# Optimization experiments

Hardware: AMD Instinct MI355X
Metric: run time of the kernel (lower is better)

## Reference

```python
import jax, jax.numpy as jnp
import numpy as np

B, T, E = 8, 1024, 512
H = 1024            # hidden_dim
NH, QD, VD = 4, 256, 512
C1, C2 = 512, 2     # conv1_out, conv2_out
K, PAD = 3, 1


def conv1d(x, w, b, pad):
    # x: [B, Cin, T], w: [Cout, Cin, K]
    y = jax.lax.conv_general_dilated(x, w, (1,), [(pad, pad)],
                                     dimension_numbers=('NCH', 'OIH', 'NCH'))
    return y + b[None, :, None]


def setup_inputs() -> dict:
    key = jax.random.key(0)
    ks = jax.random.split(key, 24)
    n = lambda i, shape, s=0.02: jax.random.normal(ks[i], shape, dtype=jnp.float32) * s
    inp = {
        'x':    jax.random.normal(ks[0], (B, T, E), dtype=jnp.float32),
        # in_pro: two 1x1 convs over channels (acting as linears)
        'w_in1': n(1, (E, E)), 'b_in1': jnp.zeros((E,), jnp.float32),
        'w_in2': n(2, (E, E)), 'b_in2': jnp.zeros((E,), jnp.float32),
        # attention projections
        'w_q': n(3, (NH * QD, E), float(np.sqrt(2.0 / (E + QD)))), 'b_q': jnp.zeros((NH * QD,), jnp.float32),
        'w_k': n(4, (NH * QD, E), float(np.sqrt(2.0 / (E + QD)))), 'b_k': jnp.zeros((NH * QD,), jnp.float32),
        'w_v': n(5, (NH * VD, E), float(np.sqrt(2.0 / (E + VD)))), 'b_v': jnp.zeros((NH * VD,), jnp.float32),
        # output projection (1x1 conv)
        'w_p': n(6, (E, NH * VD)), 'b_p': jnp.zeros((E,), jnp.float32),
        # layernorm
        'ln_g': jnp.ones((E,), jnp.float32), 'ln_b': jnp.zeros((E,), jnp.float32),
        # LSTM (1 layer, unidirectional, hidden H)
        'w_ih': n(7, (4 * H, E)), 'w_hh': n(8, (4 * H, H)),
        'b_ih': jnp.zeros((4 * H,), jnp.float32), 'b_hh': jnp.zeros((4 * H,), jnp.float32),
        # attention pooling convs
        'w_c1': n(9, (C1, H, K)), 'b_c1': jnp.zeros((C1,), jnp.float32),
        'w_c2': n(10, (C2, C1, K)), 'b_c2': jnp.zeros((C2,), jnp.float32),
    }
    return inp


def reference(x, w_in1, b_in1, w_in2, b_in2, w_q, b_q, w_k, b_k, w_v, b_v,
              w_p, b_p, ln_g, ln_b, w_ih, w_hh, b_ih, b_hh,
              w_c1, b_c1, w_c2, b_c2):
    # in_pro: 1x1 conv -> LeakyReLU(0.25) -> 1x1 conv (channel-wise linears)
    h = jnp.einsum('bte,fe->btf', x, w_in1) + b_in1
    h = jnp.where(h >= 0, h, 0.25 * h)
    h = jnp.einsum('bte,fe->btf', h, w_in2) + b_in2  # [B,T,E]

    # multi-head attention (no scale factor, as in the source)
    q = (jnp.einsum('bte,fe->btf', h, w_q) + b_q).reshape(B, T, NH, QD)
    k = (jnp.einsum('bte,fe->btf', h, w_k) + b_k).reshape(B, T, NH, QD)
    v = (jnp.einsum('bte,fe->btf', h, w_v) + b_v).reshape(B, T, NH, VD)
    scores = jnp.einsum('btnd,bsnd->bnts', q, k)          # [B,NH,T,T]
    attn = jax.nn.softmax(scores, axis=-1)
    o = jnp.einsum('bnts,bsnd->btnd', attn, v)            # [B,T,NH,VD]
    o = o.reshape(B, T, NH * VD)

    # p_conv1 (1x1) then LayerNorm over E
    y = jnp.einsum('btc,ec->bte', o, w_p) + b_p           # [B,T,E]
    mu = jnp.mean(y, axis=-1, keepdims=True)
    var = jnp.mean(jnp.square(y - mu), axis=-1, keepdims=True)
    y = (y - mu) * jax.lax.rsqrt(var + 1e-5) * ln_g + ln_b

    # LSTM (batch_first, 1 layer); dropout is identity in eval mode
    def step(carry, xt):
        hprev, cprev = carry
        g = xt @ w_ih.T + hprev @ w_hh.T + b_ih + b_hh    # [B,4H]
        i, f, gg, og = jnp.split(g, 4, axis=-1)
        c = jax.nn.sigmoid(f) * cprev + jax.nn.sigmoid(i) * jnp.tanh(gg)
        hn = jax.nn.sigmoid(og) * jnp.tanh(c)
        return (hn, c), hn
    init = (jnp.zeros((B, H), y.dtype), jnp.zeros((B, H), y.dtype))
    _, hs = jax.lax.scan(step, init, jnp.swapaxes(y, 0, 1))  # [T,B,H]
    lstm_out = jnp.swapaxes(hs, 0, 1)                        # [B,T,H]

    # conv-based attention pooling
    a = conv1d(jnp.swapaxes(lstm_out, 1, 2), w_c1, b_c1, PAD)  # [B,C1,T]
    a = jax.nn.relu(a)
    a = conv1d(a, w_c2, b_c2, PAD)                              # [B,C2,T]
    a = jax.nn.softmax(a, axis=2)
    feat = jnp.einsum('bct,bth->bch', a, lstm_out)              # [B,C2,H]
    return feat.reshape(B, C2 * H)
```

## Files before the change

### kernel.cpp

```cpp
#include <hip/hip_runtime.h>
#include <stdint.h>

typedef short short8 __attribute__((ext_vector_type(8)));
typedef short short4v __attribute__((ext_vector_type(4)));
typedef float float4v __attribute__((ext_vector_type(4)));

__device__ __forceinline__ float b2f(short s) {
    return __uint_as_float(((unsigned)(unsigned short)s) << 16);
}
__device__ __forceinline__ short f2b(float f) {
    unsigned u = __float_as_uint(f);
    unsigned r = (u + 0x7fffu + ((u >> 16) & 1u)) >> 16;
    return (short)r;
}

__global__ void k_cvt_all(const float4v* __restrict__ xs,
                          const float4v* __restrict__ s0, const float4v* __restrict__ s1,
                          const float4v* __restrict__ s2, const float4v* __restrict__ s3,
                          const float4v* __restrict__ s4, const float4v* __restrict__ s5,
                          const float4v* __restrict__ s6, const float4v* __restrict__ s7,
                          short4v* __restrict__ xq, short4v* __restrict__ wq) {
    int i = blockIdx.x * blockDim.x + threadIdx.x;
    int stride = gridDim.x * blockDim.x;
    for (; i < 3538944; i += stride) {
        float4v v;
        short4v* dst;
        int di;
        if (i < 1048576) { v = xs[i]; dst = xq; di = i; }
        else {
            int j = i - 1048576;
            dst = wq; di = j;
            if      (j <   65536) v = s0[j];
            else if (j <  131072) v = s1[j -   65536];
            else if (j <  262144) v = s2[j -  131072];
            else if (j <  393216) v = s3[j -  262144];
            else if (j <  655360) v = s4[j -  393216];
            else if (j <  917504) v = s5[j -  655360];
            else if (j < 1441792) v = s6[j -  917504];
            else                  v = s7[j - 1441792];
        }
        short4v o;
        o[0] = f2b(v[0]); o[1] = f2b(v[1]); o[2] = f2b(v[2]); o[3] = f2b(v[3]);
        dst[di] = o;
    }
}

__global__ void k_small_prep(const float* __restrict__ wc1, short* __restrict__ wc1b,
                             const float* __restrict__ bih, const float* __restrict__ bhh,
                             float* __restrict__ bsum, short* __restrict__ lpad,
                             short* __restrict__ hs0, short* __restrict__ hs1,
                             int* __restrict__ arr) {
    int t0 = blockIdx.x * blockDim.x + threadIdx.x;
    int stride = gridDim.x * blockDim.x;
    for (int i = t0; i < 512 * 3072; i += stride) {
        int c = i / 3072, rr = i % 3072, dk = rr / 1024, h = rr % 1024;
        wc1b[i] = f2b(wc1[(c * 1024 + h) * 3 + dk]);
    }
    for (int i = t0; i < 4096; i += stride) bsum[i] = bih[i] + bhh[i];
    for (int i = t0; i < 16 * 1024; i += stride) {
        int b = i >> 11, r = (i >> 10) & 1, h = i & 1023;
        lpad[((long)(b * 1026 + r * 1025)) * 1024 + h] = 0;
    }
    for (int i = t0; i < 16384; i += stride) { hs0[i] = 0; hs1[i] = 0; }
    for (int i = t0; i < 128; i += stride) arr[i] = 0;
}

__global__ __launch_bounds__(256) void k_gemm_bt(
    const short* __restrict__ A, const short* __restrict__ B,
    float* __restrict__ Cf, short* __restrict__ Cb,
    const float* __restrict__ bias,
    int M, int N, int K, int lda, int ldb, int ldc,
    int z0n, long sA0, long sA1, long sB0, long sB1, long sC0, long sC1,
    int act, int gap)
{
    __shared__ __align__(16) short lds[2 * 128 * 32];
    const int z = blockIdx.z;
    const int z0 = z % z0n, z1 = z / z0n;
    A += z1 * sA1 + z0 * sA0;
    B += z1 * sB1 + z0 * sB0;
    const long coff = z1 * sC1 + z0 * sC0;
    const int tn0 = blockIdx.x * 128, tm0 = blockIdx.y * 128;
    const int tid = threadIdx.x, ln = tid & 63, wv = tid >> 6;
    const int wr = wv >> 1, wc = wv & 1;

    const short* gbase[4];
    {
        const int gcol = (ln & 3) ^ ((ln >> 3) & 3);
#pragma unroll
        for (int j = 0; j < 4; ++j) {
            int c = wv * 4 + j;
            if (c < 8) {
                long grow = (long)(tm0 + c * 16 + (ln >> 2));
                if (gap) grow += 2 * (grow >> 10);
                gbase[j] = A + grow * (long)lda + gcol * 8;
            } else {
                gbase[j] = B + (long)(tn0 + (c - 8) * 16 + (ln >> 2)) * ldb + gcol * 8;
            }
        }
    }

    float4v acc[4][4];
#pragma unroll
    for (int i = 0; i < 4; ++i)
#pragma unroll
        for (int j = 0; j < 4; ++j) acc[i][j] = (float4v){0.f, 0.f, 0.f, 0.f};

    const int nk = K >> 5;
    for (int kt = 0; kt < nk; ++kt) {
        __syncthreads();
#pragma unroll
        for (int j = 0; j < 4; ++j) {
            int c = wv * 4 + j;
            __builtin_amdgcn_global_load_lds(
                (const __attribute__((address_space(1))) void*)(gbase[j] + kt * 32),
                (__attribute__((address_space(3))) void*)((short8*)lds + c * 64),
                16, 0, 0);
        }
        __syncthreads();

        short8 af[4], bf_[4];
        const int q = ln >> 4;
#pragma unroll
        for (int i = 0; i < 4; ++i) {
            int r = wr * 64 + i * 16 + (ln & 15);
            af[i] = ((short8*)lds)[r * 4 + (q ^ ((r >> 1) & 3))];
        }
#pragma unroll
        for (int j = 0; j < 4; ++j) {
            int r = wc * 64 + j * 16 + (ln & 15);
            bf_[j] = ((short8*)lds)[512 + r * 4 + (q ^ ((r >> 1) & 3))];
        }
#pragma unroll
        for (int i = 0; i < 4; ++i)
#pragma unroll
            for (int j = 0; j < 4; ++j)
                acc[i][j] = __builtin_amdgcn_mfma_f32_16x16x32_bf16(af[i], bf_[j], acc[i][j], 0, 0, 0);
    }

#pragma unroll
    for (int j = 0; j < 4; ++j) {
        int nglob = tn0 + wc * 64 + j * 16 + (ln & 15);
        float bv = bias ? bias[nglob] : 0.f;
#pragma unroll
        for (int i = 0; i < 4; ++i) {
#pragma unroll
            for (int r = 0; r < 4; ++r) {
                int mglob = tm0 + wr * 64 + i * 16 + (ln >> 4) * 4 + r;
                float v = acc[i][j][r] + bv;
                if (act == 1) v = (v >= 0.f) ? v : 0.25f * v;
                else if (act == 2) v = fmaxf(v, 0.f);
                long ci = coff + (long)mglob * ldc + nglob;
                if (Cf) Cf[ci] = v;
                if (Cb) Cb[ci] = f2b(v);
            }
        }
    }
}

__global__ __launch_bounds__(256) void k_gemm_bt64(
    const short* __restrict__ A, const short* __restrict__ B,
    float* __restrict__ Cf, short* __restrict__ Cb,
    const float* __restrict__ bias,
    int M, int N, int K, int lda, int ldb, int ldc,
    int z0n, long sA0, long sA1, long sB0, long sB1, long sC0, long sC1,
    int act, int gap)
{
    __shared__ __align__(16) short lds[(64 + 128) * 32];
    const int z = blockIdx.z;
    const int z0 = z % z0n, z1 = z / z0n;
    A += z1 * sA1 + z0 * sA0;
    B += z1 * sB1 + z0 * sB0;
    const long coff = z1 * sC1 + z0 * sC0;
    const int tn0 = blockIdx.x * 128, tm0 = blockIdx.y * 64;
    const int tid = threadIdx.x, ln = tid & 63, wv = tid >> 6;
    const int wr = wv >> 1, wc = wv & 1;

    const short* gbase[3];
    {
        const int gcol = (ln & 3) ^ ((ln >> 3) & 3);
#pragma unroll
        for (int j = 0; j < 3; ++j) {
            int c = wv * 3 + j;
            if (c < 4) {
                long grow = (long)(tm0 + c * 16 + (ln >> 2));
                if (gap) grow += 2 * (grow >> 10);
                gbase[j] = A + grow * (long)lda + gcol * 8;
            } else {
                gbase[j] = B + (long)(tn0 + (c - 4) * 16 + (ln >> 2)) * ldb + gcol * 8;
            }
        }
    }

    float4v acc[2][4];
#pragma unroll
    for (int i = 0; i < 2; ++i)
#pragma unroll
        for (int j = 0; j < 4; ++j) acc[i][j] = (float4v){0.f, 0.f, 0.f, 0.f};

    const int nk = K >> 5;
    for (int kt = 0; kt < nk; ++kt) {
        __syncthreads();
#pragma unroll
        for (int j = 0; j < 3; ++j) {
            int c = wv * 3 + j;
            __builtin_amdgcn_global_load_lds(
                (const __attribute__((address_space(1))) void*)(gbase[j] + kt * 32),
                (__attribute__((address_space(3))) void*)((short8*)lds + c * 64),
                16, 0, 0);
        }
        __syncthreads();

        short8 af[2], bf_[4];
        const int q = ln >> 4;
#pragma unroll
        for (int i = 0; i < 2; ++i) {
            int r = wr * 32 + i * 16 + (ln & 15);
            af[i] = ((short8*)lds)[r * 4 + (q ^ ((r >> 1) & 3))];
        }
#pragma unroll
        for (int j = 0; j < 4; ++j) {
            int r = wc * 64 + j * 16 + (ln & 15);
            bf_[j] = ((short8*)lds)[256 + r * 4 + (q ^ ((r >> 1) & 3))];
        }
#pragma unroll
        for (int i = 0; i < 2; ++i)
#pragma unroll
            for (int j = 0; j < 4; ++j)
                acc[i][j] = __builtin_amdgcn_mfma_f32_16x16x32_bf16(af[i], bf_[j], acc[i][j], 0, 0, 0);
    }

#pragma unroll
    for (int j = 0; j < 4; ++j) {
        int nglob = tn0 + wc * 64 + j * 16 + (ln & 15);
        float bv = bias ? bias[nglob] : 0.f;
#pragma unroll
        for (int i = 0; i < 2; ++i) {
#pragma unroll
            for (int r = 0; r < 4; ++r) {
                int mglob = tm0 + wr * 32 + i * 16 + (ln >> 4) * 4 + r;
                float v = acc[i][j][r] + bv;
                if (act == 1) v = (v >= 0.f) ? v : 0.25f * v;
                else if (act == 2) v = fmaxf(v, 0.f);
                long ci = coff + (long)mglob * ldc + nglob;
                if (Cf) Cf[ci] = v;
                if (Cb) Cb[ci] = f2b(v);
            }
        }
    }
}

__global__ __launch_bounds__(256) void k_softmax_rows_bf16(short* __restrict__ p) {
    long row = blockIdx.x;
    short* r = p + (row << 10);
    int tid = threadIdx.x;
    float v[4];
    float mx = -3.4e38f;
#pragma unroll
    for (int i = 0; i < 4; ++i) { v[i] = b2f(r[tid + (i << 8)]); mx = fmaxf(mx, v[i]); }
#pragma unroll
    for (int d = 32; d > 0; d >>= 1) mx = fmaxf(mx, __shfl_down(mx, d));
    __shared__ float red[4], red2[4];
    if ((tid & 63) == 0) red[tid >> 6] = mx;
    __syncthreads();
    mx = fmaxf(fmaxf(red[0], red[1]), fmaxf(red[2], red[3]));
    float s = 0.f;
#pragma unroll
    for (int i = 0; i < 4; ++i) { v[i] = __expf(v[i] - mx); s += v[i]; }
#pragma unroll
    for (int d = 32; d > 0; d >>= 1) s += __shfl_down(s, d);
    if ((tid & 63) == 0) red2[tid >> 6] = s;
    __syncthreads();
    s = red2[0] + red2[1] + red2[2] + red2[3];
    float inv = 1.f / s;
#pragma unroll
    for (int i = 0; i < 4; ++i) r[tid + (i << 8)] = f2b(v[i] * inv);
}

__global__ __launch_bounds__(256) void k_layernorm(const short* __restrict__ y,
                                                   const float* __restrict__ gam,
                                                   const float* __restrict__ bet,
                                                   short* __restrict__ o) {
    const long row = blockIdx.x;
    const short* r = y + (row << 9);
    const int tid = threadIdx.x;
    float v0 = b2f(r[tid]), v1 = b2f(r[tid + 256]);
    float s = v0 + v1, ss = v0 * v0 + v1 * v1;
#pragma unroll
    for (int d = 32; d > 0; d >>= 1) { s += __shfl_down(s, d); ss += __shfl_down(ss, d); }
    __shared__ float rs_[4], rss[4];
    if ((tid & 63) == 0) { rs_[tid >> 6] = s; rss[tid >> 6] = ss; }
    __syncthreads();
    s = rs_[0] + rs_[1] + rs_[2] + rs_[3];
    ss = rss[0] + rss[1] + rss[2] + rss[3];
    float mean = s * (1.f / 512.f);
    float var = ss * (1.f / 512.f) - mean * mean;
    float rstd = rsqrtf(var + 1e-5f);
    short* out = o + (row << 9);
    out[tid]       = f2b((v0 - mean) * rstd * gam[tid]       + bet[tid]);
    out[tid + 256] = f2b((v1 - mean) * rstd * gam[tid + 256] + bet[tid + 256]);
}

__global__ __launch_bounds__(256) void k_vT(const short* __restrict__ v, short* __restrict__ vT) {
    __shared__ short t[32][34];
    int bn = blockIdx.z, b = bn >> 2, n = bn & 3;
    int s0 = blockIdx.y * 32, d0 = blockIdx.x * 32;
    int lx = threadIdx.x & 31, ly = threadIdx.x >> 5;
#pragma unroll
    for (int i = 0; i < 4; ++i) {
        int s = ly + i * 8;
        t[s][lx] = v[(long)(b * 1024 + s0 + s) * 2048 + n * 512 + d0 + lx];
    }
    __syncthreads();
#pragma unroll
    for (int i = 0; i < 4; ++i) {
        int d = ly + i * 8;
        vT[((long)bn * 512 + d0 + d) * 1024 + s0 + lx] = t[lx][d];
    }
}

__global__ __launch_bounds__(256) void k_lstm(
    const short* __restrict__ whh, const short* __restrict__ igb,
    short* __restrict__ hA, short* __restrict__ hB,
    short* __restrict__ lstm_pad, int* __restrict__ arr)
{
    const int g = blockIdx.x;
    const int tid = threadIdx.x;
    const int ln = tid & 63, wv = tid >> 6;
    const int kbase = wv * 256 + ((ln >> 4) << 3);
    const int arow = ln & 15;

    short8 wf[4][8];
#pragma unroll
    for (int q = 0; q < 4; ++q) {
        long row = (long)q * 1024 + g * 16 + (ln & 15);
#pragma unroll
        for (int kk = 0; kk < 8; ++kk)
            wf[q][kk] = *(const short8*)&whh[row * 1024 + kbase + kk * 32];
    }

    __shared__ float part[4][16][68];
    const int gm = tid >> 4, gu = tid & 15;
    float c_prev = 0.f;
    float igv[4];
    if (tid < 128) {
#pragma unroll
        for (int q = 0; q < 4; ++q)
            igv[q] = b2f(igb[((long)gm * 1024 + 0) * 4096 + q * 1024 + g * 16 + gu]);
    }

    for (int step = 0; step < 1024; ++step) {
        const short* hp = (step & 1) ? hB : hA;
        short8 af[8];
        if (arow < 8) {
            const unsigned long long* hq =
                (const unsigned long long*)(hp + arow * 1024 + kbase);
#pragma unroll
            for (int kk = 0; kk < 8; ++kk) {
                union { unsigned long long u[2]; short8 s; } cv;
                cv.u[0] = __hip_atomic_load(hq + kk * 8,     __ATOMIC_RELAXED, __HIP_MEMORY_SCOPE_AGENT);
                cv.u[1] = __hip_atomic_load(hq + kk * 8 + 1, __ATOMIC_RELAXED, __HIP_MEMORY_SCOPE_AGENT);
                af[kk] = cv.s;
            }
        } else {
#pragma unroll
            for (int kk = 0; kk < 8; ++kk) af[kk] = (short8){0, 0, 0, 0, 0, 0, 0, 0};
        }

        float4v acc[4];
#pragma unroll
        for (int q = 0; q < 4; ++q) acc[q] = (float4v){0.f, 0.f, 0.f, 0.f};
#pragma unroll
        for (int kk = 0; kk < 8; ++kk)
#pragma unroll
            for (int q = 0; q < 4; ++q)
                acc[q] = __builtin_amdgcn_mfma_f32_16x16x32_bf16(af[kk], wf[q][kk], acc[q], 0, 0, 0);

#pragma unroll
        for (int q = 0; q < 4; ++q)
#pragma unroll
            for (int rr = 0; rr < 4; ++rr)
                part[wv][(ln >> 4) * 4 + rr][q * 16 + (ln & 15)] = acc[q][rr];
        __syncthreads();

        if (tid < 128) {
            float psum[4];
#pragma unroll
            for (int q = 0; q < 4; ++q)
                psum[q] = part[0][gm][q * 16 + gu] + part[1][gm][q * 16 + gu]
                        + part[2][gm][q * 16 + gu] + part[3][gm][q * 16 + gu];
            float g0 = psum[0] + igv[0];
            float g1 = psum[1] + igv[1];
            float g2 = psum[2] + igv[2];
            float g3 = psum[3] + igv[3];
            float iv = 1.f / (1.f + __expf(-g0));
            float fv = 1.f / (1.f + __expf(-g1));
            float gv = 2.f / (1.f + __expf(-2.f * g2)) - 1.f;
            float ov = 1.f / (1.f + __expf(-g3));
            float c = fv * c_prev + iv * gv;
            c_prev = c;
            float h = ov * (2.f / (1.f + __expf(-2.f * c)) - 1.f);
            short hb16 = f2b(h);
            short* hn = (step & 1) ? hA : hB;
            __hip_atomic_store(&hn[gm * 1024 + g * 16 + gu], hb16,
                               __ATOMIC_RELAXED, __HIP_MEMORY_SCOPE_AGENT);
            lstm_pad[((long)gm * 1026 + step + 1) * 1024 + g * 16 + gu] = hb16;
        }

        __syncthreads();
        if (tid == 0)
            __hip_atomic_store(&arr[g], step + 1, __ATOMIC_RELAXED, __HIP_MEMORY_SCOPE_AGENT);
        if (tid < 128 && step + 1 < 1024) {
#pragma unroll
            for (int q = 0; q < 4; ++q)
                igv[q] = b2f(igb[((long)gm * 1024 + step + 1) * 4096 + q * 1024 + g * 16 + gu]);
        }
        if (wv == 0) {
            const int target = step + 1;
            long att = 0;
            while (true) {
                int f0 = __hip_atomic_load(&arr[ln], __ATOMIC_RELAXED, __HIP_MEMORY_SCOPE_AGENT);
                if (__all(f0 >= target)) break;
                if (++att > 20000000L) break;
                __builtin_amdgcn_s_sleep(1);
            }
        }
        __syncthreads();
    }
}

__global__ __launch_bounds__(256) void k_conv2(const short* __restrict__ a1,
                                               const float* __restrict__ w,
                                               const float* __restrict__ bias,
                                               float* __restrict__ a2) {
    __shared__ float wl[1536];
    int blk = blockIdx.x;
    int b = blk >> 3, c = (blk >> 2) & 1, t0 = (blk & 3) * 256;
    int tid = threadIdx.x;
    for (int i = tid; i < 1536; i += 256) wl[i] = w[c * 1536 + i];
    __syncthreads();
    int t = t0 + tid;
    float s = bias[c];
    for (int dk = 0; dk < 3; ++dk) {
        int tt = t + dk - 1;
        if (tt < 0 || tt >= 1024) continue;
        const short8* arow = (const short8*)(a1 + (long)(b * 1024 + tt) * 512);
#pragma unroll 4
        for (int j = 0; j < 64; ++j) {
            short8 v = arow[j];
#pragma unroll
            for (int u = 0; u < 8; ++u)
                s += b2f(v[u]) * wl[(j * 8 + u) * 3 + dk];
        }
    }
    a2[(b * 2 + c) * 1024 + t] = s;
}

__global__ __launch_bounds__(256) void k_feat(const float* __restrict__ a2,
                                              const short* __restrict__ lstm_pad,
                                              float* __restrict__ out) {
    int blk = blockIdx.x;
    int bc = blk >> 2, qh = blk & 3;
    int b = bc >> 1;
    int tid = threadIdx.x;
    int h = qh * 256 + tid;
    __shared__ float aw[1024];
    __shared__ float red[4], red2[4];
    float v[4];
    float mx = -3.4e38f;
#pragma unroll
    for (int i = 0; i < 4; ++i) { v[i] = a2[bc * 1024 + tid + (i << 8)]; mx = fmaxf(mx, v[i]); }
#pragma unroll
    for (int d = 32; d > 0; d >>= 1) mx = fmaxf(mx, __shfl_down(mx, d));
    if ((tid & 63) == 0) red[tid >> 6] = mx;
    __syncthreads();
    mx = fmaxf(fmaxf(red[0], red[1]), fmaxf(red[2], red[3]));
    float s = 0.f;
#pragma unroll
    for (int i = 0; i < 4; ++i) { v[i] = __expf(v[i] - mx); s += v[i]; }
#pragma unroll
    for (int d = 32; d > 0; d >>= 1) s += __shfl_down(s, d);
    if ((tid & 63) == 0) red2[tid >> 6] = s;
    __syncthreads();
    s = red2[0] + red2[1] + red2[2] + red2[3];
    float inv = 1.f / s;
#pragma unroll
    for (int i = 0; i < 4; ++i) aw[tid + (i << 8)] = v[i] * inv;
    __syncthreads();
    float acc = 0.f;
#pragma unroll 16
    for (int t = 0; t < 1024; ++t)
        acc += aw[t] * b2f(lstm_pad[((long)(b * 1026 + t + 1)) * 1024 + h]);
    out[bc * 1024 + h] = acc;
}

static void gemm_bt(hipStream_t st, const short* A, const short* B, float* Cf, short* Cb,
                    const float* bias, int M, int N, int K, int lda, int ldb, int ldc,
                    int z, int z0n, long sA0, long sA1, long sB0, long sB1, long sC0, long sC1,
                    int act, int gap) {
    dim3 grid(N / 128, M / 128, z);
    k_gemm_bt<<<grid, dim3(256), 0, st>>>(A, B, Cf, Cb, bias, M, N, K, lda, ldb, ldc,
                                          z0n, sA0, sA1, sB0, sB1, sC0, sC1, act, gap);
}

static void gemm_bt64(hipStream_t st, const short* A, const short* B, float* Cf, short* Cb,
                      const float* bias, int M, int N, int K, int lda, int ldb, int ldc,
                      int z, int z0n, long sA0, long sA1, long sB0, long sB1, long sC0, long sC1,
                      int act, int gap) {
    dim3 grid(N / 128, M / 64, z);
    k_gemm_bt64<<<grid, dim3(256), 0, st>>>(A, B, Cf, Cb, bias, M, N, K, lda, ldb, ldc,
                                            z0n, sA0, sA1, sB0, sB1, sC0, sC1, act, gap);
}

extern "C" void kernel_launch(void* const* d_in, const int* in_sizes, int n_in,
                              void* d_out, int out_size, void* d_ws, size_t ws_size,
                              hipStream_t stream) {
    if (ws_size < 199409920u) return;

    const float* x     = (const float*)d_in[0];
    const float* w_in1 = (const float*)d_in[1];
    const float* b_in1 = (const float*)d_in[2];
    const float* w_in2 = (const float*)d_in[3];
    const float* b_in2 = (const float*)d_in[4];
    const float* w_q   = (const float*)d_in[5];
    const float* b_q   = (const float*)d_in[6];
    const float* w_k   = (const float*)d_in[7];
    const float* b_k   = (const float*)d_in[8];
    const float* w_v   = (const float*)d_in[9];
    const float* b_v   = (const float*)d_in[10];
    const float* w_p   = (const float*)d_in[11];
    const float* b_p   = (const float*)d_in[12];
    const float* ln_g  = (const float*)d_in[13];
    const float* ln_b  = (const float*)d_in[14];
    const float* w_ih  = (const float*)d_in[15];
    const float* w_hh  = (const float*)d_in[16];
    const float* b_ih  = (const float*)d_in[17];
    const float* b_hh  = (const float*)d_in[18];
    const float* w_c1  = (const float*)d_in[19];
    const float* b_c1  = (const float*)d_in[20];
    const float* w_c2  = (const float*)d_in[21];
    const float* b_c2  = (const float*)d_in[22];

    char* ws = (char*)d_ws;
    short* w1b  = (short*)(ws + 0);
    short* w2b  = (short*)(ws + 524288);
    short* wqb  = (short*)(ws + 1048576);
    short* wkb  = (short*)(ws + 2097152);
    short* wvb  = (short*)(ws + 3145728);
    short* wpb  = (short*)(ws + 5242880);
    short* wihb = (short*)(ws + 7340032);
    short* whhb = (short*)(ws + 11534336);
    short* wc1b = (short*)(ws + 19922944);
    float* bsum = (float*)(ws + 23068672);
    short* hs0  = (short*)(ws + 23085056);
    short* hs1  = (short*)(ws + 23117824);
    int*   arr  = (int*)  (ws + 23150592);
    float* a2   = (float*)(ws + 23150848);
    short* lpad = (short*)(ws + 23216384);
    const size_t D0 = 40026368u;
    short* xbf   = (short*)(ws + D0);
    short* h1bf  = (short*)(ws + D0 + 8388608);
    short* h2bf  = (short*)(ws + D0 + 16777216);
    short* qbf   = (short*)(ws + D0 + 25165824);
    short* kbf   = (short*)(ws + D0 + 41943040);
    short* vbf   = (short*)(ws + D0 + 58720256);
    short* vTbf  = (short*)(ws + D0 + 92274688);
    short* scb   = (short*)(ws + D0 + 58720256);
    short* obf   = (short*)(ws + D0 + 125829120);
    short* ybf   = (short*)(ws + D0 + 58720256);
    short* ylnbf = (short*)(ws + D0 + 67108864);
    short* igb   = (short*)(ws + D0 + 92274688);
    short* a1bf  = (short*)(ws + D0);

    k_cvt_all<<<dim3(4096), dim3(256), 0, stream>>>(
        (const float4v*)x,
        (const float4v*)w_in1, (const float4v*)w_in2, (const float4v*)w_q, (const float4v*)w_k,
        (const float4v*)w_v, (const float4v*)w_p, (const float4v*)w_ih, (const float4v*)w_hh,
        (short4v*)xbf, (short4v*)w1b);
    k_small_prep<<<dim3(128), dim3(256), 0, stream>>>(
        w_c1, wc1b, b_ih, b_hh, bsum, lpad, hs0, hs1, arr);

    gemm_bt64(stream, xbf, w1b, nullptr, h1bf, b_in1, 8192, 512, 512, 512, 512, 512,
              1, 1, 0, 0, 0, 0, 0, 0, 1, 0);
    gemm_bt64(stream, h1bf, w2b, nullptr, h2bf, b_in2, 8192, 512, 512, 512, 512, 512,
              1, 1, 0, 0, 0, 0, 0, 0, 0, 0);
    gemm_bt64(stream, h2bf, wqb, nullptr, qbf, b_q, 8192, 1024, 512, 512, 512, 1024,
              1, 1, 0, 0, 0, 0, 0, 0, 0, 0);
    gemm_bt64(stream, h2bf, wkb, nullptr, kbf, b_k, 8192, 1024, 512, 512, 512, 1024,
              1, 1, 0, 0, 0, 0, 0, 0, 0, 0);
    gemm_bt(stream, h2bf, wvb, nullptr, vbf, b_v, 8192, 2048, 512, 512, 512, 2048,
            1, 1, 0, 0, 0, 0, 0, 0, 0, 0);
    k_vT<<<dim3(16, 32, 32), dim3(256), 0, stream>>>(vbf, vTbf);

    for (int bg = 0; bg < 2; ++bg) {
        const short* qb = qbf + (long)bg * 4194304;
        const short* kb = kbf + (long)bg * 4194304;
        gemm_bt(stream, qb, kb, nullptr, scb, nullptr, 1024, 1024, 256, 1024, 1024, 1024,
                16, 4, 256, 1048576, 256, 1048576, 1048576, 4194304, 0, 0);
        k_softmax_rows_bf16<<<dim3(16384), dim3(256), 0, stream>>>(scb);
        gemm_bt64(stream, scb, vTbf + (long)bg * 8388608, nullptr, obf + (long)bg * 8388608, nullptr,
                  1024, 512, 1024, 1024, 1024, 2048,
                  16, 4, 1048576, 4194304, 524288, 2097152, 512, 2097152, 0, 0);
    }

    gemm_bt64(stream, obf, wpb, nullptr, ybf, b_p, 8192, 512, 2048, 2048, 2048, 512,
              1, 1, 0, 0, 0, 0, 0, 0, 0, 0);
    k_layernorm<<<dim3(8192), dim3(256), 0, stream>>>(ybf, ln_g, ln_b, ylnbf);
    gemm_bt(stream, ylnbf, wihb, nullptr, igb, bsum, 8192, 4096, 512, 512, 512, 4096,
            1, 1, 0, 0, 0, 0, 0, 0, 0, 0);
    k_lstm<<<dim3(64), dim3(256), 0, stream>>>(whhb, igb, hs0, hs1, lpad, arr);
    gemm_bt64(stream, lpad, wc1b, nullptr, a1bf, b_c1, 8192, 512, 3072, 1024, 3072, 512,
              1, 1, 0, 0, 0, 0, 0, 0, 2, 1);
    k_conv2<<<dim3(64), dim3(256), 0, stream>>>(a1bf, w_c2, b_c2, a2);
    k_feat<<<dim3(64), dim3(256), 0, stream>>>(a2, lpad, (float*)d_out);
    (void)in_sizes; (void)n_in; (void)out_size; (void)ws_size;
}
```

Baseline: 3.965 ms.

## Fuse Q/K projections, split-K conv1 GEMM, and widen conv2/feat grids with atomics

Q and K projections are merged into one GEMM over a concatenated weight, using a second bias for the upper half of the output columns, and the attention score GEMM now reads from the interleaved QK buffer. The conv1 GEMM after the LSTM is split over K into two fp32 partial outputs, which a new kernel sums with bias and ReLU. conv2 and feat are spread over four times as many blocks, each handling a slice and accumulating with atomicAdd into zero- or bias-initialised buffers. This aims to cut launch count and raise occupancy on the small tail kernels, at the cost of extra fp32 partial traffic and atomics whose summation order is nondeterministic.

```diff
diff --git a/kernel.cpp b/kernel.cpp
--- a/kernel.cpp
+++ b/kernel.cpp
@@ -49,7 +49,8 @@
                              const float* __restrict__ bih, const float* __restrict__ bhh,
                              float* __restrict__ bsum, short* __restrict__ lpad,
                              short* __restrict__ hs0, short* __restrict__ hs1,
-                             int* __restrict__ arr) {
+                             int* __restrict__ arr, const float* __restrict__ bc2,
+                             float* __restrict__ a2) {
     int t0 = blockIdx.x * blockDim.x + threadIdx.x;
     int stride = gridDim.x * blockDim.x;
     for (int i = t0; i < 512 * 3072; i += stride) {
@@ -62,7 +63,8 @@
         lpad[((long)(b * 1026 + r * 1025)) * 1024 + h] = 0;
     }
     for (int i = t0; i < 16384; i += stride) { hs0[i] = 0; hs1[i] = 0; }
-    for (int i = t0; i < 128; i += stride) arr[i] = 0;
+    for (int i = t0; i < 64; i += stride) arr[i] = 0;
+    for (int i = t0; i < 16384; i += stride) a2[i] = bc2[(i >> 10) & 1];
 }
 
 __global__ __launch_bounds__(256) void k_gemm_bt(
@@ -71,7 +73,7 @@
     const float* __restrict__ bias,
     int M, int N, int K, int lda, int ldb, int ldc,
     int z0n, long sA0, long sA1, long sB0, long sB1, long sC0, long sC1,
-    int act, int gap)
+    int act, int gap, const float* __restrict__ bias2, int nsplit)
 {
     __shared__ __align__(16) short lds[2 * 128 * 32];
     const int z = blockIdx.z;
@@ -140,7 +142,8 @@
 #pragma unroll
     for (int j = 0; j < 4; ++j) {
         int nglob = tn0 + wc * 64 + j * 16 + (ln & 15);
-        float bv = bias ? bias[nglob] : 0.f;
+        float bv = 0.f;
+        if (bias) bv = (bias2 && nglob >= nsplit) ? bias2[nglob - nsplit] : bias[nglob];
 #pragma unroll
         for (int i = 0; i < 4; ++i) {
 #pragma unroll
@@ -163,7 +166,7 @@
     const float* __restrict__ bias,
     int M, int N, int K, int lda, int ldb, int ldc,
     int z0n, long sA0, long sA1, long sB0, long sB1, long sC0, long sC1,
-    int act, int gap)
+    int act, int gap, const float* __restrict__ bias2, int nsplit)
 {
     __shared__ __align__(16) short lds[(64 + 128) * 32];
     const int z = blockIdx.z;
@@ -232,7 +235,8 @@
 #pragma unroll
     for (int j = 0; j < 4; ++j) {
         int nglob = tn0 + wc * 64 + j * 16 + (ln & 15);
-        float bv = bias ? bias[nglob] : 0.f;
+        float bv = 0.f;
+        if (bias) bv = (bias2 && nglob >= nsplit) ? bias2[nglob - nsplit] : bias[nglob];
 #pragma unroll
         for (int i = 0; i < 2; ++i) {
 #pragma unroll
@@ -246,6 +250,24 @@
                 if (Cb) Cb[ci] = f2b(v);
             }
         }
+    }
+}
+
+__global__ __launch_bounds__(256) void k_comb1(const float4v* __restrict__ p0,
+                                               const float4v* __restrict__ p1,
+                                               const float* __restrict__ bias,
+                                               short4v* __restrict__ o) {
+    int i = blockIdx.x * blockDim.x + threadIdx.x;
+    int stride = gridDim.x * blockDim.x;
+    for (; i < 1048576; i += stride) {
+        float4v a = p0[i], b = p1[i];
+        short4v r;
+#pragma unroll
+        for (int u = 0; u < 4; ++u) {
+            float v = a[u] + b[u] + bias[(i * 4 + u) & 511];
+            r[u] = f2b(fmaxf(v, 0.f));
+        }
+        o[i] = r;
     }
 }
 
@@ -430,40 +452,44 @@
 
 __global__ __launch_bounds__(256) void k_conv2(const short* __restrict__ a1,
                                                const float* __restrict__ w,
-                                               const float* __restrict__ bias,
-                                               float* __restrict__ a2) {
-    __shared__ float wl[1536];
+                                               float* __restrict__ a2,
+                                               float* __restrict__ dz) {
+    __shared__ float wl[384];
     int blk = blockIdx.x;
-    int b = blk >> 3, c = (blk >> 2) & 1, t0 = (blk & 3) * 256;
+    int chunk = blk & 3, tq = (blk >> 2) & 3, bc = blk >> 4;
+    int b = bc >> 1, c = bc & 1, t0 = tq * 256;
     int tid = threadIdx.x;
-    for (int i = tid; i < 1536; i += 256) wl[i] = w[c * 1536 + i];
+    int gid = blk * 256 + tid;
+    if (gid < 16384) dz[gid] = 0.f;
+    for (int i = tid; i < 384; i += 256) wl[i] = w[c * 1536 + chunk * 384 + i];
     __syncthreads();
     int t = t0 + tid;
-    float s = bias[c];
+    int j0 = chunk * 16;
+    float s = 0.f;
     for (int dk = 0; dk < 3; ++dk) {
         int tt = t + dk - 1;
         if (tt < 0 || tt >= 1024) continue;
         const short8* arow = (const short8*)(a1 + (long)(b * 1024 + tt) * 512);
 #pragma unroll 4
-        for (int j = 0; j < 64; ++j) {
-            short8 v = arow[j];
+        for (int j = 0; j < 16; ++j) {
+            short8 v = arow[j0 + j];
 #pragma unroll
             for (int u = 0; u < 8; ++u)
                 s += b2f(v[u]) * wl[(j * 8 + u) * 3 + dk];
         }
     }
-    a2[(b * 2 + c) * 1024 + t] = s;
+    atomicAdd(&a2[(b * 2 + c) * 1024 + t], s);
 }
 
 __global__ __launch_bounds__(256) void k_feat(const float* __restrict__ a2,
                                               const short* __restrict__ lstm_pad,
                                               float* __restrict__ out) {
     int blk = blockIdx.x;
-    int bc = blk >> 2, qh = blk & 3;
+    int tc = blk & 3, qh = (blk >> 2) & 3, bc = blk >> 4;
     int b = bc >> 1;
     int tid = threadIdx.x;
     int h = qh * 256 + tid;
-    __shared__ float aw[1024];
+    __shared__ float aws[256];
     __shared__ float red[4], red2[4];
     float v[4];
     float mx = -3.4e38f;
@@ -483,32 +509,31 @@
     __syncthreads();
     s = red2[0] + red2[1] + red2[2] + red2[3];
     float inv = 1.f / s;
-#pragma unroll
-    for (int i = 0; i < 4; ++i) aw[tid + (i << 8)] = v[i] * inv;
+    aws[tid] = v[tc] * inv;
     __syncthreads();
     float acc = 0.f;
 #pragma unroll 16
-    for (int t = 0; t < 1024; ++t)
-        acc += aw[t] * b2f(lstm_pad[((long)(b * 1026 + t + 1)) * 1024 + h]);
-    out[bc * 1024 + h] = acc;
+    for (int j = 0; j < 256; ++j)
+        acc += aws[j] * b2f(lstm_pad[((long)(b * 1026 + tc * 256 + j + 1)) * 1024 + h]);
+    atomicAdd(&out[bc * 1024 + h], acc);
 }
 
 static void gemm_bt(hipStream_t st, const short* A, const short* B, float* Cf, short* Cb,
                     const float* bias, int M, int N, int K, int lda, int ldb, int ldc,
                     int z, int z0n, long sA0, long sA1, long sB0, long sB1, long sC0, long sC1,
-                    int act, int gap) {
+                    int act, int gap, const float* bias2 = nullptr, int nsplit = 0) {
     dim3 grid(N / 128, M / 128, z);
     k_gemm_bt<<<grid, dim3(256), 0, st>>>(A, B, Cf, Cb, bias, M, N, K, lda, ldb, ldc,
-                                          z0n, sA0, sA1, sB0, sB1, sC0, sC1, act, gap);
+                                          z0n, sA0, sA1, sB0, sB1, sC0, sC1, act, gap, bias2, nsplit);
 }
 
 static void gemm_bt64(hipStream_t st, const short* A, const short* B, float* Cf, short* Cb,
                       const float* bias, int M, int N, int K, int lda, int ldb, int ldc,
                       int z, int z0n, long sA0, long sA1, long sB0, long sB1, long sC0, long sC1,
-                      int act, int gap) {
+                      int act, int gap, const float* bias2 = nullptr, int nsplit = 0) {
     dim3 grid(N / 128, M / 64, z);
     k_gemm_bt64<<<grid, dim3(256), 0, st>>>(A, B, Cf, Cb, bias, M, N, K, lda, ldb, ldc,
-                                            z0n, sA0, sA1, sB0, sB1, sC0, sC1, act, gap);
+                                            z0n, sA0, sA1, sB0, sB1, sC0, sC1, act, gap, bias2, nsplit);
 }
 
 extern "C" void kernel_launch(void* const* d_in, const int* in_sizes, int n_in,
@@ -544,7 +569,6 @@
     short* w1b  = (short*)(ws + 0);
     short* w2b  = (short*)(ws + 524288);
     short* wqb  = (short*)(ws + 1048576);
-    short* wkb  = (short*)(ws + 2097152);
     short* wvb  = (short*)(ws + 3145728);
     short* wpb  = (short*)(ws + 5242880);
     short* wihb = (short*)(ws + 7340032);
@@ -560,8 +584,7 @@
     short* xbf   = (short*)(ws + D0);
     short* h1bf  = (short*)(ws + D0 + 8388608);
     short* h2bf  = (short*)(ws + D0 + 16777216);
-    short* qbf   = (short*)(ws + D0 + 25165824);
-    short* kbf   = (short*)(ws + D0 + 41943040);
+    short* qkC   = (short*)(ws + D0 + 25165824);
     short* vbf   = (short*)(ws + D0 + 58720256);
     short* vTbf  = (short*)(ws + D0 + 92274688);
     short* scb   = (short*)(ws + D0 + 58720256);
@@ -570,6 +593,8 @@
     short* ylnbf = (short*)(ws + D0 + 67108864);
     short* igb   = (short*)(ws + D0 + 92274688);
     short* a1bf  = (short*)(ws + D0);
+    float* cp0   = (float*)(ws + D0 + 8388608);
+    float* cp1   = (float*)(ws + D0 + 25165824);
 
     k_cvt_all<<<dim3(4096), dim3(256), 0, stream>>>(
         (const float4v*)x,
@@ -577,25 +602,23 @@
         (const float4v*)w_v, (const float4v*)w_p, (const float4v*)w_ih, (const float4v*)w_hh,
         (short4v*)xbf, (short4v*)w1b);
     k_small_prep<<<dim3(128), dim3(256), 0, stream>>>(
-        w_c1, wc1b, b_ih, b_hh, bsum, lpad, hs0, hs1, arr);
+        w_c1, wc1b, b_ih, b_hh, bsum, lpad, hs0, hs1, arr, b_c2, a2);
 
     gemm_bt64(stream, xbf, w1b, nullptr, h1bf, b_in1, 8192, 512, 512, 512, 512, 512,
               1, 1, 0, 0, 0, 0, 0, 0, 1, 0);
     gemm_bt64(stream, h1bf, w2b, nullptr, h2bf, b_in2, 8192, 512, 512, 512, 512, 512,
               1, 1, 0, 0, 0, 0, 0, 0, 0, 0);
-    gemm_bt64(stream, h2bf, wqb, nullptr, qbf, b_q, 8192, 1024, 512, 512, 512, 1024,
-              1, 1, 0, 0, 0, 0, 0, 0, 0, 0);
-    gemm_bt64(stream, h2bf, wkb, nullptr, kbf, b_k, 8192, 1024, 512, 512, 512, 1024,
-              1, 1, 0, 0, 0, 0, 0, 0, 0, 0);
+    gemm_bt(stream, h2bf, wqb, nullptr, qkC, b_q, 8192, 2048, 512, 512, 512, 2048,
+            1, 1, 0, 0, 0, 0, 0, 0, 0, 0, b_k, 1024);
     gemm_bt(stream, h2bf, wvb, nullptr, vbf, b_v, 8192, 2048, 512, 512, 512, 2048,
             1, 1, 0, 0, 0, 0, 0, 0, 0, 0);
     k_vT<<<dim3(16, 32, 32), dim3(256), 0, stream>>>(vbf, vTbf);
 
     for (int bg = 0; bg < 2; ++bg) {
-        const short* qb = qbf + (long)bg * 4194304;
-        const short* kb = kbf + (long)bg * 4194304;
-        gemm_bt(stream, qb, kb, nullptr, scb, nullptr, 1024, 1024, 256, 1024, 1024, 1024,
-                16, 4, 256, 1048576, 256, 1048576, 1048576, 4194304, 0, 0);
+        const short* qb = qkC + (long)bg * 8388608;
+        const short* kb = qkC + 1024 + (long)bg * 8388608;
+        gemm_bt(stream, qb, kb, nullptr, scb, nullptr, 1024, 1024, 256, 2048, 2048, 1024,
+                16, 4, 256, 2097152, 256, 2097152, 1048576, 4194304, 0, 0);
         k_softmax_rows_bf16<<<dim3(16384), dim3(256), 0, stream>>>(scb);
         gemm_bt64(stream, scb, vTbf + (long)bg * 8388608, nullptr, obf + (long)bg * 8388608, nullptr,
                   1024, 512, 1024, 1024, 1024, 2048,
@@ -608,9 +631,11 @@
     gemm_bt(stream, ylnbf, wihb, nullptr, igb, bsum, 8192, 4096, 512, 512, 512, 4096,
             1, 1, 0, 0, 0, 0, 0, 0, 0, 0);
     k_lstm<<<dim3(64), dim3(256), 0, stream>>>(whhb, igb, hs0, hs1, lpad, arr);
-    gemm_bt64(stream, lpad, wc1b, nullptr, a1bf, b_c1, 8192, 512, 3072, 1024, 3072, 512,
-              1, 1, 0, 0, 0, 0, 0, 0, 2, 1);
-    k_conv2<<<dim3(64), dim3(256), 0, stream>>>(a1bf, w_c2, b_c2, a2);
-    k_feat<<<dim3(64), dim3(256), 0, stream>>>(a2, lpad, (float*)d_out);
+    gemm_bt64(stream, lpad, wc1b, cp0, nullptr, nullptr, 8192, 512, 1536, 1024, 3072, 512,
+              2, 2, 1536, 0, 1536, 0, 4194304, 0, 0, 1);
+    k_comb1<<<dim3(4096), dim3(256), 0, stream>>>(
+        (const float4v*)cp0, (const float4v*)cp1, b_c1, (short4v*)a1bf);
+    k_conv2<<<dim3(256), dim3(256), 0, stream>>>(a1bf, w_c2, a2, (float*)d_out);
+    k_feat<<<dim3(256), dim3(256), 0, stream>>>(a2, lpad, (float*)d_out);
     (void)in_sizes; (void)n_in; (void)out_size; (void)ws_size;
 }
```

Measured after the change: 3.905 ms. No clear change (-1.5%).
